# Kernel tuning notes

Measured on AMD Instinct MI355X. Metric: run time of the kernel, lower is better.

The kernel has to match this reference:

```python
import jax, jax.numpy as jnp
import numpy as np
import math

DIM = 1024
NUM_HEADS = 16
HEAD_DIM = DIM // NUM_HEADS
ROPE_BASE = 10000.0


def _rope_cos_sin(seq_len, head_dim, dtype):
    inv_freq = 1.0 / (ROPE_BASE ** (jnp.arange(0, head_dim, 2, dtype=jnp.float32) / head_dim))
    t = jnp.arange(seq_len, dtype=jnp.float32)
    freqs = jnp.einsum('i,j->ij', t, inv_freq)          # (S, head_dim/2)
    emb = jnp.concatenate([freqs, freqs], axis=-1)      # (S, head_dim)
    return jnp.cos(emb).astype(dtype), jnp.sin(emb).astype(dtype)


def _rotate_half(x):
    x1, x2 = jnp.split(x, 2, axis=-1)
    return jnp.concatenate([-x2, x1], axis=-1)


def setup_inputs() -> dict:
    key = jax.random.key(0)
    kx, kq, kk, kv, ko = jax.random.split(key, 5)
    B, S = 4, 2048
    scale = 1.0 / math.sqrt(DIM)
    x = jax.random.normal(kx, (B, S, DIM), dtype=jnp.float32)
    Wq = jax.random.normal(kq, (DIM, DIM), dtype=jnp.float32) * scale
    Wk = jax.random.normal(kk, (DIM, DIM), dtype=jnp.float32) * scale
    Wv = jax.random.normal(kv, (DIM, DIM), dtype=jnp.float32) * scale
    Wo = jax.random.normal(ko, (DIM, DIM), dtype=jnp.float32) * scale
    mask = jnp.tril(jnp.ones((S, S), dtype=jnp.int32))  # causal mask
    return {"x": x, "Wq": Wq, "Wk": Wk, "Wv": Wv, "Wo": Wo, "mask": mask}


def reference(x, Wq, Wk, Wv, Wo, mask):
    B, S, _ = x.shape
    # projections (nn.Linear: y = x @ W.T)
    def split_heads(t):
        return t.reshape(B, S, NUM_HEADS, HEAD_DIM).transpose(0, 2, 1, 3)  # (B,H,S,D)
    q = split_heads(x @ Wq.T)
    k = split_heads(x @ Wk.T)
    v = split_heads(x @ Wv.T)
    # RoPE
    cos, sin = _rope_cos_sin(S, HEAD_DIM, x.dtype)      # (S, D)
    cos = cos[None, None]; sin = sin[None, None]
    q = q * cos + _rotate_half(q) * sin
    k = k * cos + _rotate_half(k) * sin
    # attention
    scores = jnp.einsum('bhsd,bhtd->bhst', q, k) / math.sqrt(HEAD_DIM)
    neg_inf = jnp.asarray(-jnp.inf, dtype=scores.dtype)
    scores = jnp.where(mask[None, None] == 0, neg_inf, scores)
    attn = jax.nn.softmax(scores, axis=-1)
    out = jnp.einsum('bhst,bhtd->bhsd', attn, v)        # (B,H,S,D)
    out = out.transpose(0, 2, 1, 3).reshape(B, S, DIM)
    return out @ Wo.T
```

## Files before the change

### kernel.cpp

```cpp
#include <hip/hip_runtime.h>
#include <hip/hip_bf16.h>

#define BDIM 1024
#define NH 16
#define HD 64
#define BB 4
#define SS 2048
#define MTOT (BB*SS)
#define NT (SS/64)

typedef __bf16 bf16x8 __attribute__((ext_vector_type(8)));
typedef float f32x4 __attribute__((ext_vector_type(4)));

__device__ __forceinline__ unsigned short f2b(float f){
    __bf16 h = (__bf16)f;
    return __builtin_bit_cast(unsigned short, h);
}

__device__ __forceinline__ void ld16(const unsigned short* g, unsigned short* l){
    __builtin_amdgcn_global_load_lds(
        (const __attribute__((address_space(1))) unsigned int*)(const void*)g,
        (__attribute__((address_space(3))) unsigned int*)(void*)l, 16, 0, 0);
}

__global__ void setup_all(const float* __restrict__ x,
                          const float* __restrict__ Wq, const float* __restrict__ Wk,
                          const float* __restrict__ Wv, const float* __restrict__ Wo,
                          unsigned short* __restrict__ xb,
                          unsigned short* __restrict__ oq, unsigned short* __restrict__ ok,
                          unsigned short* __restrict__ ov, unsigned short* __restrict__ oo,
                          float2* __restrict__ rt){
    const int bid = blockIdx.x;
    const int tid = threadIdx.x;
    if (bid < 8192){
        int i = bid * 256 + tid;
        float4 v = ((const float4*)x)[i];
        ushort4 o;
        o.x = f2b(v.x); o.y = f2b(v.y); o.z = f2b(v.z); o.w = f2b(v.w);
        ((ushort4*)xb)[i] = o;
    } else if (bid < 12288){
        int idx = bid - 8192;
        int which = idx >> 10;
        const float* in = (which == 0) ? Wq : (which == 1) ? Wk : (which == 2) ? Wv : Wo;
        unsigned short* out = (which == 0) ? oq : (which == 1) ? ok : (which == 2) ? ov : oo;
        int i = (idx & 1023) * 256 + tid;
        float4 v = ((const float4*)in)[i];
        ushort4 o;
        o.x = f2b(v.x); o.y = f2b(v.y); o.z = f2b(v.z); o.w = f2b(v.w);
        ((ushort4*)out)[i] = o;
    } else {
        int i = (bid - 12288) * 256 + tid;
        int s = i >> 5, d = i & 31;
        float theta = (float)s * exp2f(-0.41524101186092029f * (float)d);
        float sn, c;
        sincosf(theta, &sn, &c);
        rt[i] = make_float2(c, sn);
    }
}

__device__ __forceinline__ void gemm_mainloop(
    const unsigned short* __restrict__ A,
    const unsigned short* __restrict__ Bw,
    unsigned short* At, unsigned short* Bt,
    f32x4 acc[4][4], int m0, int n0)
{
    const int tid  = threadIdx.x;
    const int lane = tid & 63;
    const int wave = tid >> 6;
    const int wr = wave >> 1, wc = wave & 1;
    const int lh = lane >> 4, ll = lane & 15;
    const int K = 1024;

    for (int k0 = 0; k0 < K; k0 += 64){
        #pragma unroll
        for (int c = 0; c < 4; ++c){
            int g   = c*256 + tid;
            int row = g >> 3;
            int off = (g & 7) * 8;
            int base = (c*256 + wave*64) * 8;
            ld16(A  + (size_t)(m0+row)*K + k0 + off, At + base);
            ld16(Bw + (size_t)(n0+row)*K + k0 + off, Bt + base);
        }
        __syncthreads();
        #pragma unroll
        for (int ks = 0; ks < 2; ++ks){
            bf16x8 af[4], bfr[4];
            #pragma unroll
            for (int i = 0; i < 4; ++i)
                af[i] = *(const bf16x8*)(At + (wr*64 + i*16 + ll)*64 + ks*32 + lh*8);
            #pragma unroll
            for (int j = 0; j < 4; ++j)
                bfr[j] = *(const bf16x8*)(Bt + (wc*64 + j*16 + ll)*64 + ks*32 + lh*8);
            #pragma unroll
            for (int i = 0; i < 4; ++i)
                #pragma unroll
                for (int j = 0; j < 4; ++j)
                    acc[i][j] = __builtin_amdgcn_mfma_f32_16x16x32_bf16(af[i], bfr[j], acc[i][j], 0, 0, 0);
        }
        __syncthreads();
    }
}

#define TILE_US 4096

__global__ __launch_bounds__(256, 2) void gemm_qkv(
    const unsigned short* __restrict__ Xb,
    const unsigned short* __restrict__ Wq,
    const unsigned short* __restrict__ Wk,
    const unsigned short* __restrict__ Wv,
    const float2* __restrict__ Rt,
    unsigned short* __restrict__ Qt,
    unsigned short* __restrict__ Kt,
    unsigned short* __restrict__ VTt)
{
    __shared__ alignas(16) unsigned short At[128*64];
    __shared__ alignas(16) unsigned short Bt[128*64];
    const int z = blockIdx.z;
    const unsigned short* Bw = (z == 0) ? Wq : (z == 1 ? Wk : Wv);
    const int m0 = blockIdx.y * 128, n0 = blockIdx.x * 128;
    f32x4 acc[4][4] = {};
    gemm_mainloop(Xb, Bw, At, Bt, acc, m0, n0);

    const int lane = threadIdx.x & 63;
    const int wave = threadIdx.x >> 6;
    const int wr = wave >> 1, wc = wave & 1;
    const int lh = lane >> 4, ll = lane & 15;
    const int h  = blockIdx.x*2 + wc;
    const int b  = m0 >> 11;
    const int bh = b*NH + h;

    if (z < 2){
        const float qs = (z == 0) ? 0.125f * 1.44269504f : 1.0f;
        unsigned short* C = (z == 0) ? Qt : Kt;
        #pragma unroll
        for (int i = 0; i < 4; ++i)
            #pragma unroll
            for (int r = 0; r < 4; ++r){
                int m = m0 + wr*64 + i*16 + lh*4 + r;
                int s = m & (SS-1);
                int kt = s >> 6;
                const float2* rowcs = Rt + (s << 5);
                size_t fb = ((size_t)(bh*NT + kt)*8 + i)*512 + (size_t)(lh*4 + r)*8;
                #pragma unroll
                for (int jl = 0; jl < 2; ++jl){
                    int d_lo = jl*16 + ll;
                    float2 cs = rowcs[d_lo];
                    float a_lo = acc[i][jl][r], a_hi = acc[i][jl+2][r];
                    float y_lo = (a_lo*cs.x - a_hi*cs.y) * qs;
                    float y_hi = (a_hi*cs.x + a_lo*cs.y) * qs;
                    size_t off = fb + (size_t)(jl*2 + (ll>>3))*128 + (ll&7);
                    C[off]        = f2b(y_lo);
                    C[off + 2048] = f2b(y_hi);
                }
            }
    } else {
        const int s0 = (m0 & (SS-1)) + wr*64;
        const int kt = s0 >> 6;
        #pragma unroll
        for (int i = 0; i < 4; ++i)
            #pragma unroll
            for (int j = 0; j < 4; ++j){
                unsigned short tmp[4];
                #pragma unroll
                for (int r = 0; r < 4; ++r)
                    tmp[r] = f2b(acc[i][j][r]);
                size_t off = ((size_t)(bh*NT + kt)*8 + (i>>1)*4 + j)*512
                           + (size_t)(((i&1)*2 + (lh>>1))*16 + ll)*8 + (lh&1)*4;
                *(uint2*)(VTt + off) = *(const uint2*)tmp;
            }
    }
}

__global__ __launch_bounds__(256, 2) void gemm_out(
    const unsigned short* __restrict__ Ab,
    const unsigned short* __restrict__ Wo,
    float* __restrict__ Cout)
{
    __shared__ alignas(16) unsigned short At[128*64];
    __shared__ alignas(16) unsigned short Bt[128*64];
    const int m0 = blockIdx.y * 128, n0 = blockIdx.x * 128;
    f32x4 acc[4][4] = {};
    gemm_mainloop(Ab, Wo, At, Bt, acc, m0, n0);

    const int lane = threadIdx.x & 63;
    const int wave = threadIdx.x >> 6;
    const int wr = wave >> 1, wc = wave & 1;
    const int lh = lane >> 4, ll = lane & 15;
    #pragma unroll
    for (int i = 0; i < 4; ++i)
        #pragma unroll
        for (int j = 0; j < 4; ++j)
            #pragma unroll
            for (int r = 0; r < 4; ++r){
                int m = m0 + wr*64 + i*16 + lh*4 + r;
                int n = n0 + wc*64 + j*16 + ll;
                Cout[(size_t)m*BDIM + n] = acc[i][j][r];
            }
}

__device__ __forceinline__ void attn_tile(
    const bf16x8 qf[2], bool diag, int ws, int lane, int lh, int ll,
    const unsigned short* Ksh, const unsigned short* Vsh, unsigned short* Prow,
    float li[4], f32x4 o[4])
{
    f32x4 sc[4] = {};
    #pragma unroll
    for (int ks = 0; ks < 2; ++ks)
        #pragma unroll
        for (int j = 0; j < 4; ++j){
            bf16x8 bfr = *(const bf16x8*)(Ksh + (ks*4 + j)*512 + lane*8);
            sc[j] = __builtin_amdgcn_mfma_f32_16x16x32_bf16(qf[ks], bfr, sc[j], 0, 0, 0);
        }
    if (diag){
        #pragma unroll
        for (int j = 0; j < 4; ++j){
            int key = j*16 + ll;
            #pragma unroll
            for (int r = 0; r < 4; ++r){
                int qrow = ws*16 + lh*4 + r;
                if (key > qrow) sc[j][r] = -1e30f;
            }
        }
    }
    #pragma unroll
    for (int j = 0; j < 4; ++j)
        #pragma unroll
        for (int r = 0; r < 4; ++r)
            sc[j][r] = exp2f(sc[j][r] - 28.0f);
    #pragma unroll
    for (int r = 0; r < 4; ++r)
        li[r] += (sc[0][r] + sc[1][r]) + (sc[2][r] + sc[3][r]);
    #pragma unroll
    for (int j = 0; j < 4; ++j)
        #pragma unroll
        for (int r = 0; r < 4; ++r)
            Prow[(lh*4 + r)*72 + j*16 + ll] = f2b(sc[j][r]);
    #pragma unroll
    for (int ks = 0; ks < 2; ++ks){
        bf16x8 pf = *(const bf16x8*)(Prow + ll*72 + ks*32 + lh*8);
        #pragma unroll
        for (int t = 0; t < 4; ++t){
            bf16x8 vf = *(const bf16x8*)(Vsh + (ks*4 + t)*512 + lane*8);
            o[t] = __builtin_amdgcn_mfma_f32_16x16x32_bf16(pf, vf, o[t], 0, 0, 0);
        }
    }
}

__device__ __forceinline__ void store_o(
    unsigned short* S, const f32x4 o[4], const float li[4],
    int lane, int lh, int ll, int q0w, int b, int h,
    unsigned short* __restrict__ Obuf)
{
    #pragma unroll
    for (int r = 0; r < 4; ++r){
        float inv = 1.0f / li[r];
        #pragma unroll
        for (int t = 0; t < 4; ++t)
            S[(lh*4 + r)*72 + t*16 + ll] = f2b(o[t][r] * inv);
    }
    int row = lane >> 2, c4 = (lane & 3) * 8;
    size_t rb = ((size_t)(b*SS + q0w + row))*BDIM + h*HD;
    *(uint4*)(Obuf + rb + c4)      = *(uint4*)(S + row*72 + c4);
    *(uint4*)(Obuf + rb + 32 + c4) = *(uint4*)(S + row*72 + 32 + c4);
}

__global__ __launch_bounds__(512, 4) void attn_kernel(
    const unsigned short* __restrict__ Qt,
    const unsigned short* __restrict__ Kt,
    const unsigned short* __restrict__ VTt,
    unsigned short* __restrict__ Obuf)
{
    __shared__ alignas(16) unsigned short Ksh[TILE_US];
    __shared__ alignas(16) unsigned short Vsh[TILE_US];
    __shared__ alignas(16) unsigned short Psh[8][16*72];

    const int tid  = threadIdx.x;
    const int lane = tid & 63;
    const int wave = tid >> 6;
    const int grp  = wave >> 2;
    const int ws   = wave & 3;
    const int lh = lane >> 4, ll = lane & 15;
    const int bx = blockIdx.x;
    const int bh = blockIdx.y;

    const int tS = (grp == 0) ? bx        : 15 - bx;
    const int tL = (grp == 0) ? NT-1 - bx : 16 + bx;
    const int ktMax = NT-1 - bx;

    const unsigned short* Qhf = Qt  + (size_t)bh * NT * TILE_US;
    const unsigned short* Khf = Kt  + (size_t)bh * NT * TILE_US;
    const unsigned short* Vhf = VTt + (size_t)bh * NT * TILE_US;

    bf16x8 qfS[2], qfL[2];
    #pragma unroll
    for (int ks = 0; ks < 2; ++ks){
        qfS[ks] = *(const bf16x8*)(Qhf + (size_t)(tS*8 + ks*4 + ws)*512 + lane*8);
        qfL[ks] = *(const bf16x8*)(Qhf + (size_t)(tL*8 + ks*4 + ws)*512 + lane*8);
    }

    f32x4 oS[4] = {}, oL[4] = {};
    float liS[4] = {0.f,0.f,0.f,0.f}, liL[4] = {0.f,0.f,0.f,0.f};

    const int tb = tid * 8;

    uint4 kr = *(const uint4*)(Khf + tb);
    uint4 vr = *(const uint4*)(Vhf + tb);

    for (int kt = 0; kt <= ktMax; ++kt){
        __syncthreads();
        *(uint4*)(Ksh + tb) = kr;
        *(uint4*)(Vsh + tb) = vr;
        __syncthreads();
        if (kt < ktMax){
            size_t nb = (size_t)(kt + 1) * TILE_US + tb;
            kr = *(const uint4*)(Khf + nb);
            vr = *(const uint4*)(Vhf + nb);
        }
        if (kt <= tL)
            attn_tile(qfL, kt == tL, ws, lane, lh, ll, Ksh, Vsh, Psh[wave], liL, oL);
        if (kt <= tS)
            attn_tile(qfS, kt == tS, ws, lane, lh, ll, Ksh, Vsh, Psh[wave], liS, oS);
    }

    #pragma unroll
    for (int r = 0; r < 4; ++r){
        float sS = liS[r], sL = liL[r];
        #pragma unroll
        for (int x = 1; x < 16; x <<= 1){
            sS += __shfl_xor(sS, x);
            sL += __shfl_xor(sL, x);
        }
        liS[r] = sS; liL[r] = sL;
    }

    int b = bh >> 4, h = bh & 15;
    store_o(Psh[wave], oS, liS, lane, lh, ll, tS*64 + ws*16, b, h, Obuf);
    store_o(Psh[wave], oL, liL, lane, lh, ll, tL*64 + ws*16, b, h, Obuf);
}

extern "C" void kernel_launch(void* const* d_in, const int* in_sizes, int n_in,
                              void* d_out, int out_size, void* d_ws, size_t ws_size,
                              hipStream_t stream) {
    const float* x  = (const float*)d_in[0];
    const float* Wq = (const float*)d_in[1];
    const float* Wk = (const float*)d_in[2];
    const float* Wv = (const float*)d_in[3];
    const float* Wo = (const float*)d_in[4];

    char* w = (char*)d_ws;
    unsigned short* xb  = (unsigned short*)(w);
    unsigned short* wqb = (unsigned short*)(w + (16u  << 20));
    unsigned short* wkb = (unsigned short*)(w + (18u  << 20));
    unsigned short* wvb = (unsigned short*)(w + (20u  << 20));
    unsigned short* wob = (unsigned short*)(w + (22u  << 20));
    unsigned short* Qt  = (unsigned short*)(w + (24u  << 20));
    unsigned short* Kt  = (unsigned short*)(w + (40u  << 20));
    unsigned short* VTt = (unsigned short*)(w + (56u  << 20));
    unsigned short* Ob  = (unsigned short*)(w + (72u  << 20));
    float2*         Rt  = (float2*)(w + (88u << 20));

    setup_all<<<12544, 256, 0, stream>>>(x, Wq, Wk, Wv, Wo, xb, wqb, wkb, wvb, wob, Rt);

    gemm_qkv<<<dim3(8, 64, 3), 256, 0, stream>>>(xb, wqb, wkb, wvb, Rt, Qt, Kt, VTt);
    attn_kernel<<<dim3(8, 64), 512, 0, stream>>>(Qt, Kt, VTt, Ob);
    gemm_out<<<dim3(8, 64), 256, 0, stream>>>(Ob, wob, (float*)d_out);
}
```

Baseline: 284.1 us.

## Split attention work into one query tile per wave group, doubling grid

```diff
diff --git a/kernel.cpp b/kernel.cpp
--- a/kernel.cpp
+++ b/kernel.cpp
@@ -283,23 +283,20 @@
     const int bx = blockIdx.x;
     const int bh = blockIdx.y;
 
-    const int tS = (grp == 0) ? bx        : 15 - bx;
-    const int tL = (grp == 0) ? NT-1 - bx : 16 + bx;
-    const int ktMax = NT-1 - bx;
+    const int myT   = 2*bx + grp;
+    const int ktMax = 2*bx + 1;
 
     const unsigned short* Qhf = Qt  + (size_t)bh * NT * TILE_US;
     const unsigned short* Khf = Kt  + (size_t)bh * NT * TILE_US;
     const unsigned short* Vhf = VTt + (size_t)bh * NT * TILE_US;
 
-    bf16x8 qfS[2], qfL[2];
-    #pragma unroll
-    for (int ks = 0; ks < 2; ++ks){
-        qfS[ks] = *(const bf16x8*)(Qhf + (size_t)(tS*8 + ks*4 + ws)*512 + lane*8);
-        qfL[ks] = *(const bf16x8*)(Qhf + (size_t)(tL*8 + ks*4 + ws)*512 + lane*8);
-    }
-
-    f32x4 oS[4] = {}, oL[4] = {};
-    float liS[4] = {0.f,0.f,0.f,0.f}, liL[4] = {0.f,0.f,0.f,0.f};
+    bf16x8 qf[2];
+    #pragma unroll
+    for (int ks = 0; ks < 2; ++ks)
+        qf[ks] = *(const bf16x8*)(Qhf + (size_t)(myT*8 + ks*4 + ws)*512 + lane*8);
+
+    f32x4 o[4] = {};
+    float li[4] = {0.f,0.f,0.f,0.f};
 
     const int tb = tid * 8;
 
@@ -316,26 +313,21 @@
             kr = *(const uint4*)(Khf + nb);
             vr = *(const uint4*)(Vhf + nb);
         }
-        if (kt <= tL)
-            attn_tile(qfL, kt == tL, ws, lane, lh, ll, Ksh, Vsh, Psh[wave], liL, oL);
-        if (kt <= tS)
-            attn_tile(qfS, kt == tS, ws, lane, lh, ll, Ksh, Vsh, Psh[wave], liS, oS);
+        if (kt <= myT)
+            attn_tile(qf, kt == myT, ws, lane, lh, ll, Ksh, Vsh, Psh[wave], li, o);
     }
 
     #pragma unroll
     for (int r = 0; r < 4; ++r){
-        float sS = liS[r], sL = liL[r];
-        #pragma unroll
-        for (int x = 1; x < 16; x <<= 1){
-            sS += __shfl_xor(sS, x);
-            sL += __shfl_xor(sL, x);
-        }
-        liS[r] = sS; liL[r] = sL;
+        float s = li[r];
+        #pragma unroll
+        for (int x = 1; x < 16; x <<= 1)
+            s += __shfl_xor(s, x);
+        li[r] = s;
     }
 
     int b = bh >> 4, h = bh & 15;
-    store_o(Psh[wave], oS, liS, lane, lh, ll, tS*64 + ws*16, b, h, Obuf);
-    store_o(Psh[wave], oL, liL, lane, lh, ll, tL*64 + ws*16, b, h, Obuf);
+    store_o(Psh[wave], o, li, lane, lh, ll, myT*64 + ws*16, b, h, Obuf);
 }
 
 extern "C" void kernel_launch(void* const* d_in, const int* in_sizes, int n_in,
@@ -362,6 +354,6 @@
     setup_all<<<12544, 256, 0, stream>>>(x, Wq, Wk, Wv, Wo, xb, wqb, wkb, wvb, wob, Rt);
 
     gemm_qkv<<<dim3(8, 64, 3), 256, 0, stream>>>(xb, wqb, wkb, wvb, Rt, Qt, Kt, VTt);
-    attn_kernel<<<dim3(8, 64), 512, 0, stream>>>(Qt, Kt, VTt, Ob);
+    attn_kernel<<<dim3(16, 64), 512, 0, stream>>>(Qt, Kt, VTt, Ob);
     gemm_out<<<dim3(8, 64), 256, 0, stream>>>(Ob, wob, (float*)d_out);
 }
```

After: 329.4 us. +16.0%, slower.
